# Optimization experiments

Measured on AMD Instinct MI355X. Metric: run time of the kernel, lower is better.

Reference implementation:

```python
import jax, jax.numpy as jnp
import numpy as np

VNUM = 50000
OUT = 128
E = 1600000
EPS = 1e-7


def setup_inputs() -> dict:
    key = jax.random.key(0)
    k = jax.random.split(key, 8)
    sidx = jax.random.randint(k[0], (E,), 0, VNUM, dtype=jnp.int64 if jax.config.jax_enable_x64 else jnp.int32)
    tidx = jax.random.randint(k[1], (E,), 0, VNUM, dtype=sidx.dtype)
    enorm = jax.random.uniform(k[2], (E,), dtype=jnp.float32)
    # edge signs +-1 as in signed graph conv
    esgn = jnp.where(jax.random.uniform(k[3], (E,)) < 0.5, -1.0, 1.0).astype(jnp.float32)
    # vrepr initialized trunc_normal(std=0.1) (zero_init=False)
    vrepr = 0.1 * jax.random.truncated_normal(k[4], -2.0, 2.0, (VNUM, OUT), dtype=jnp.float32)
    lim = 1.0 / np.sqrt(OUT)
    loc_w = jax.random.uniform(k[5], (OUT, OUT), jnp.float32, -lim, lim)
    loc_b = jnp.zeros((OUT,), jnp.float32)
    std_w = jax.random.uniform(k[6], (OUT, OUT), jnp.float32, -lim, lim)
    std_b = jnp.zeros((OUT,), jnp.float32)
    return {"sidx": sidx, "tidx": tidx, "enorm": enorm, "esgn": esgn,
            "vrepr": vrepr, "loc_w": loc_w, "loc_b": loc_b,
            "std_w": std_w, "std_b": std_b}


def reference(sidx, tidx, enorm, esgn, vrepr, loc_w, loc_b, std_w, std_b):
    # GraphConv: edge-weighted gather + scatter-add aggregation
    msg = vrepr[sidx] * (esgn * enorm)[:, None]          # [E, OUT]
    ptr = jax.ops.segment_sum(msg, tidx, num_segments=VNUM)  # [VNUM, OUT]
    loc = ptr @ loc_w.T + loc_b                          # Normal loc
    std = jax.nn.softplus(ptr @ std_w.T + std_b) + EPS   # Normal scale
    return loc, std
```

## Files before the change

kernel.cpp:

```cpp
#include <hip/hip_runtime.h>
#include <math.h>

#define VNUM 50000
#define OUTF 128
#define NEDGE 1600000
#define EPSF 1e-7f

#define CONV_BLOCKS 6250
#define BFRAG_BLOCKS 64

#define CHUNK 2048
#define NCB 49
#define COARSE_BLOCKS 782
#define BSTRIDE 36864
#define NSUB 4
#define FINE_BLOCKS (NCB * NSUB)

typedef __attribute__((ext_vector_type(8))) short short8;
typedef __attribute__((ext_vector_type(4))) float v4f;

__device__ __forceinline__ unsigned short f2bf(float f) {
    union { float f; unsigned int u; } c; c.f = f;
    unsigned int u = c.u;
    return (unsigned short)((u + 0x7FFFu + ((u >> 16) & 1u)) >> 16);
}
__device__ __forceinline__ float bf16_lo(unsigned int p) {
    union { unsigned int u; float f; } c; c.u = p << 16; return c.f;
}
__device__ __forceinline__ float bf16_hi(unsigned int p) {
    union { unsigned int u; float f; } c; c.u = p & 0xFFFF0000u; return c.f;
}

__device__ __forceinline__ int wave_incl_scan(int v, int lane) {
#pragma unroll
    for (int off = 1; off < 64; off <<= 1) {
        const int o = __shfl_up(v, off, 64);
        if (lane >= off) v += o;
    }
    return v;
}

__global__ __launch_bounds__(256) void prep_kernel(
    const float* __restrict__ vrepr, unsigned int* __restrict__ vrepr16,
    int* __restrict__ ccursor,
    const float* __restrict__ loc_w, const float* __restrict__ std_w,
    unsigned int* bfrag)
{
    const int b = blockIdx.x, tid = threadIdx.x;
    if (b < CONV_BLOCKS) {
        const size_t base = (size_t)b * 1024 + tid * 4;
        const float4 v = *reinterpret_cast<const float4*>(vrepr + base);
        uint2 o;
        o.x = (unsigned)f2bf(v.x) | ((unsigned)f2bf(v.y) << 16);
        o.y = (unsigned)f2bf(v.z) | ((unsigned)f2bf(v.w) << 16);
        *reinterpret_cast<uint2*>(vrepr16 + base / 2) = o;
    } else if (b == CONV_BLOCKS) {
        if (tid < NCB) ccursor[tid] = tid * BSTRIDE;
    } else {
        const int p = (b - (CONV_BLOCKS + 1)) * 256 + tid;
        const int j2 = p & 3, lq = (p >> 2) & 63, ks = (p >> 8) & 3, ct = p >> 10;
        const int k = ks * 32 + (lq >> 4) * 8 + j2 * 2;
        const int n = ct * 16 + (lq & 15);
        const float* wsrc = (n >> 7) ? std_w : loc_w;
        const int c = n & 127;
        bfrag[p] = (unsigned)f2bf(wsrc[c * 128 + k]) |
                   ((unsigned)f2bf(wsrc[c * 128 + k + 1]) << 16);
    }
}

__global__ __launch_bounds__(256) void coarse_kernel(
    const int* __restrict__ sidx, const int* __restrict__ tidx,
    const float* __restrict__ enorm, const float* __restrict__ esgn,
    int* __restrict__ ccursor, uint2* __restrict__ coarse8)
{
    __shared__ uint2 lrec[CHUNK];
    __shared__ int lcnt[4][NCB];
    __shared__ int lbase[4][NCB];
    __shared__ int loffs[NCB];
    __shared__ int grun[NCB];

    const int tid = threadIdx.x, lane = tid & 63, wv = tid >> 6;
    const int base = blockIdx.x * CHUNK;
    const int n = min(CHUNK, NEDGE - base);

    for (int i = tid; i < 4 * NCB; i += 256) (&lcnt[0][0])[i] = 0;
    __syncthreads();

    uint2 rec[8];
#pragma unroll
    for (int j = 0; j < 8; ++j) {
        const int e = base + j * 256 + tid;
        if (e < NEDGE) {
            const int t = tidx[e];
            const float w = esgn[e] * enorm[e];
            rec[j].x = ((unsigned)sidx[e] << 16) | (unsigned)f2bf(w);
            rec[j].y = (unsigned)t;
            atomicAdd(&lcnt[wv][t >> 10], 1);
        }
    }
    __syncthreads();

    if (tid < 64) {
        int c0 = 0, c1 = 0, c2 = 0, c3 = 0, tot = 0;
        if (lane < NCB) {
            c0 = lcnt[0][lane]; c1 = lcnt[1][lane];
            c2 = lcnt[2][lane]; c3 = lcnt[3][lane];
            tot = c0 + c1 + c2 + c3;
        }
        const int inc = wave_incl_scan(tot, lane);
        const int ex = inc - tot;
        if (lane < NCB) {
            loffs[lane]    = ex;
            lbase[0][lane] = ex;
            lbase[1][lane] = ex + c0;
            lbase[2][lane] = ex + c0 + c1;
            lbase[3][lane] = ex + c0 + c1 + c2;
            grun[lane] = atomicAdd(&ccursor[lane], tot);
        }
    }
    __syncthreads();

#pragma unroll
    for (int j = 0; j < 8; ++j) {
        const int e = base + j * 256 + tid;
        if (e < NEDGE) {
            const int cb = (int)(rec[j].y >> 10);
            const int pos = atomicAdd(&lbase[wv][cb], 1);
            lrec[pos] = rec[j];
        }
    }
    __syncthreads();

    for (int i = tid; i < n; i += 256) {
        const uint2 r = lrec[i];
        const int cb = (int)(r.y >> 10);
        coarse8[grun[cb] + (i - loffs[cb])] = r;
    }
}

__global__ __launch_bounds__(64) void scan_mid_kernel(
    const int* __restrict__ ccursor, int* __restrict__ cbase,
    int* __restrict__ offs)
{
    const int tid = threadIdx.x;
    const int len = (tid < NCB) ? (ccursor[tid] - tid * BSTRIDE) : 0;
    const int inc = wave_incl_scan(len, tid);
    const int ex = inc - len;
    if (tid < NCB) cbase[tid] = ex;
    if (tid == NCB - 1) { cbase[NCB] = inc; offs[VNUM] = inc; }
}

__global__ __launch_bounds__(1024) void hist_kernel(
    const uint2* __restrict__ coarse8, const int* __restrict__ cbase,
    int* __restrict__ hcnt)
{
    __shared__ int cnt[1024];
    const int tid = threadIdx.x;
    const int bin = blockIdx.x >> 2, s = blockIdx.x & 3;
    const int bs = bin * BSTRIDE;
    const int len = cbase[bin + 1] - cbase[bin];
    const int qs = bs + ((len * s) >> 2);
    const int qe = bs + ((len * (s + 1)) >> 2);
    cnt[tid] = 0;
    __syncthreads();
    for (int i = qs + tid; i < qe; i += 1024)
        atomicAdd(&cnt[coarse8[i].y & 1023], 1);
    __syncthreads();
    hcnt[blockIdx.x * 1024 + tid] = cnt[tid];
}

__global__ __launch_bounds__(1024) void scatter_fine_kernel(
    const uint2* __restrict__ coarse8, const int* __restrict__ cbase,
    const int* __restrict__ hcnt, int* __restrict__ offs,
    unsigned int* __restrict__ pairs)
{
    __shared__ int cur[1024];
    __shared__ int wsum[16];
    const int tid = threadIdx.x, lane = tid & 63, wv = tid >> 6;
    const int bin = blockIdx.x >> 2, s = blockIdx.x & 3;
    const int bs = bin * BSTRIDE;
    const int s0 = cbase[bin];
    const int len = cbase[bin + 1] - s0;
    const int qs = bs + ((len * s) >> 2);
    const int qe = bs + ((len * (s + 1)) >> 2);

    const int c0 = hcnt[(bin * 4 + 0) * 1024 + tid];
    const int c1 = hcnt[(bin * 4 + 1) * 1024 + tid];
    const int c2 = hcnt[(bin * 4 + 2) * 1024 + tid];
    const int c3 = hcnt[(bin * 4 + 3) * 1024 + tid];
    const int tot = c0 + c1 + c2 + c3;
    const int pre = (s > 0 ? c0 : 0) + (s > 1 ? c1 : 0) + (s > 2 ? c2 : 0);

    const int inc = wave_incl_scan(tot, lane);
    if (lane == 63) wsum[wv] = inc;
    __syncthreads();
    if (tid == 0) {
        int run = 0;
        for (int i = 0; i < 16; ++i) { const int t = wsum[i]; wsum[i] = run; run += t; }
    }
    __syncthreads();
    const int ex = s0 + wsum[wv] + inc - tot;
    const int gv = (bin << 10) + tid;
    if (s == 0 && gv < VNUM) offs[gv] = ex;
    cur[tid] = ex + pre;
    __syncthreads();

    for (int i = qs + tid; i < qe; i += 1024) {
        const uint2 r = coarse8[i];
        const int pos = atomicAdd(&cur[r.y & 1023], 1);
        pairs[pos] = r.x;
    }
}

__global__ __launch_bounds__(256) void aggregate_kernel(
    const int* __restrict__ offs, const unsigned int* __restrict__ pairs,
    const unsigned int* __restrict__ vrepr16, float* __restrict__ acc)
{
    const int v = blockIdx.x * 4 + (threadIdx.x >> 6);
    const int l = threadIdx.x & 63;
    int i = offs[v];
    const int end = offs[v + 1];

    float a0 = 0.0f, a1 = 0.0f;
    for (; i + 12 <= end; i += 12) {
        unsigned p[12], r[12];
#pragma unroll
        for (int j = 0; j < 12; ++j) p[j] = pairs[i + j];
#pragma unroll
        for (int j = 0; j < 12; ++j) r[j] = vrepr16[(size_t)(p[j] >> 16) * 64 + l];
#pragma unroll
        for (int j = 0; j < 12; ++j) {
            const float w = bf16_lo(p[j]);
            a0 = fmaf(bf16_lo(r[j]), w, a0);
            a1 = fmaf(bf16_hi(r[j]), w, a1);
        }
    }
    for (; i + 8 <= end; i += 8) {
        unsigned p[8], r[8];
#pragma unroll
        for (int j = 0; j < 8; ++j) p[j] = pairs[i + j];
#pragma unroll
        for (int j = 0; j < 8; ++j) r[j] = vrepr16[(size_t)(p[j] >> 16) * 64 + l];
#pragma unroll
        for (int j = 0; j < 8; ++j) {
            const float w = bf16_lo(p[j]);
            a0 = fmaf(bf16_lo(r[j]), w, a0);
            a1 = fmaf(bf16_hi(r[j]), w, a1);
        }
    }
    for (; i + 4 <= end; i += 4) {
        const unsigned p0 = pairs[i], p1 = pairs[i + 1];
        const unsigned p2 = pairs[i + 2], p3 = pairs[i + 3];
        const unsigned r0 = vrepr16[(size_t)(p0 >> 16) * 64 + l];
        const unsigned r1 = vrepr16[(size_t)(p1 >> 16) * 64 + l];
        const unsigned r2 = vrepr16[(size_t)(p2 >> 16) * 64 + l];
        const unsigned r3 = vrepr16[(size_t)(p3 >> 16) * 64 + l];
        const float w0 = bf16_lo(p0), w1 = bf16_lo(p1);
        const float w2 = bf16_lo(p2), w3 = bf16_lo(p3);
        a0 = fmaf(bf16_lo(r0), w0, a0); a1 = fmaf(bf16_hi(r0), w0, a1);
        a0 = fmaf(bf16_lo(r1), w1, a0); a1 = fmaf(bf16_hi(r1), w1, a1);
        a0 = fmaf(bf16_lo(r2), w2, a0); a1 = fmaf(bf16_hi(r2), w2, a1);
        a0 = fmaf(bf16_lo(r3), w3, a0); a1 = fmaf(bf16_hi(r3), w3, a1);
    }
    for (; i < end; ++i) {
        const unsigned p = pairs[i];
        const unsigned r = vrepr16[(size_t)(p >> 16) * 64 + l];
        const float w = bf16_lo(p);
        a0 = fmaf(bf16_lo(r), w, a0); a1 = fmaf(bf16_hi(r), w, a1);
    }
    *reinterpret_cast<float2*>(acc + (size_t)v * OUTF + 2 * l) = make_float2(a0, a1);
}

__global__ __launch_bounds__(256) void gemm_mfma_kernel(
    const float* acc, const unsigned int* __restrict__ bfrag,
    const float* __restrict__ loc_b, const float* __restrict__ std_b,
    float* out)
{
    __shared__ unsigned short tile[16][136];
    const int t = threadIdx.x;
    const int row0 = blockIdx.x * 16;
    const int l = t & 63, w = t >> 6;

    short8 bfr[4][4];
#pragma unroll
    for (int ct = 0; ct < 4; ++ct)
#pragma unroll
        for (int ks = 0; ks < 4; ++ks)
            bfr[ct][ks] = *reinterpret_cast<const short8*>(
                bfrag + ((((w * 4 + ct) * 4 + ks) * 64 + l) << 2));

    {
        const float* src = acc + (size_t)row0 * OUTF + t * 8;
        const float4 v0 = *reinterpret_cast<const float4*>(src);
        const float4 v1 = *reinterpret_cast<const float4*>(src + 4);
        uint4 pk;
        pk.x = (unsigned)f2bf(v0.x) | ((unsigned)f2bf(v0.y) << 16);
        pk.y = (unsigned)f2bf(v0.z) | ((unsigned)f2bf(v0.w) << 16);
        pk.z = (unsigned)f2bf(v1.x) | ((unsigned)f2bf(v1.y) << 16);
        pk.w = (unsigned)f2bf(v1.z) | ((unsigned)f2bf(v1.w) << 16);
        *reinterpret_cast<uint4*>(&tile[t >> 4][(t & 15) * 8]) = pk;
    }
    __syncthreads();

    const int m = l & 15, q = l >> 4;
    v4f accv[4];
#pragma unroll
    for (int ct = 0; ct < 4; ++ct) accv[ct] = (v4f){0.0f, 0.0f, 0.0f, 0.0f};

#pragma unroll
    for (int ks = 0; ks < 4; ++ks) {
        const short8 a = *reinterpret_cast<const short8*>(&tile[m][ks * 32 + q * 8]);
#pragma unroll
        for (int ct = 0; ct < 4; ++ct)
            accv[ct] = __builtin_amdgcn_mfma_f32_16x16x32_bf16(
                a, bfr[ct][ks], accv[ct], 0, 0, 0);
    }

#pragma unroll
    for (int ct = 0; ct < 4; ++ct) {
        const int colg = (w * 4 + ct) * 16 + m;
        const int h = colg >> 7, c = colg & 127;
        const float bias = (h ? std_b : loc_b)[c];
        float* dst = out + (h ? (size_t)VNUM * OUTF : (size_t)0);
#pragma unroll
        for (int reg = 0; reg < 4; ++reg) {
            const int row = row0 + q * 4 + reg;
            float x = accv[ct][reg] + bias;
            if (h) x = fmaxf(x, 0.0f) + log1pf(expf(-fabsf(x))) + EPSF;
            dst[(size_t)row * OUTF + c] = x;
        }
    }
}

__global__ __launch_bounds__(256) void gemm_fallback_kernel(
    const float* acc,
    const float* __restrict__ loc_w, const float* __restrict__ loc_b,
    const float* __restrict__ std_w, const float* __restrict__ std_b,
    float* out)
{
    __shared__ float tile[16][OUTF];
    const int t = threadIdx.x;
    const int row0 = blockIdx.x * 16;
    {
        const float4* src = reinterpret_cast<const float4*>(acc + (size_t)row0 * OUTF);
        float4* dst = reinterpret_cast<float4*>(&tile[0][0]);
        dst[t] = src[t]; dst[t + 256] = src[t + 256];
    }
    __syncthreads();
    const int is_std = t >> 7;
    const int c = t & 127;
    const float* w = (is_std ? std_w : loc_w) + (size_t)c * OUTF;
    const float bias = is_std ? std_b[c] : loc_b[c];
    float accv[16];
#pragma unroll
    for (int r = 0; r < 16; ++r) accv[r] = 0.0f;
    for (int k = 0; k < OUTF; k += 4) {
        const float4 wv = *reinterpret_cast<const float4*>(w + k);
#pragma unroll
        for (int r = 0; r < 16; ++r) {
            const float4 pv = *reinterpret_cast<const float4*>(&tile[r][k]);
            float a = accv[r];
            a = fmaf(pv.x, wv.x, a); a = fmaf(pv.y, wv.y, a);
            a = fmaf(pv.z, wv.z, a); a = fmaf(pv.w, wv.w, a);
            accv[r] = a;
        }
    }
    float* dst_base = out + (is_std ? (size_t)VNUM * OUTF : (size_t)0);
#pragma unroll
    for (int r = 0; r < 16; ++r) {
        const float x = accv[r] + bias;
        dst_base[(size_t)(row0 + r) * OUTF + c] =
            is_std ? (fmaxf(x, 0.0f) + log1pf(expf(-fabsf(x))) + EPSF) : x;
    }
}

extern "C" void kernel_launch(void* const* d_in, const int* in_sizes, int n_in,
                              void* d_out, int out_size, void* d_ws, size_t ws_size,
                              hipStream_t stream) {
    const int*   sidx  = (const int*)  d_in[0];
    const int*   tidx  = (const int*)  d_in[1];
    const float* enorm = (const float*)d_in[2];
    const float* esgn  = (const float*)d_in[3];
    const float* vrepr = (const float*)d_in[4];
    const float* loc_w = (const float*)d_in[5];
    const float* loc_b = (const float*)d_in[6];
    const float* std_w = (const float*)d_in[7];
    const float* std_b = (const float*)d_in[8];

    float* out = (float*)d_out;

    uint2* coarse8 = (uint2*)out;

    unsigned int* sbase   = (unsigned int*)(out + (size_t)VNUM * OUTF);
    unsigned int* pairs   = sbase;
    unsigned int* vrepr16 = sbase + NEDGE;
    int* offs    = (int*)(sbase + NEDGE + (size_t)VNUM * 64);
    int* cbase   = offs + VNUM + 1;
    int* ccursor = cbase + NCB + 1;
    int* hcnt    = ccursor + NCB;

    const bool use_ws = ws_size >= 16384 * sizeof(unsigned int);
    unsigned int* bfrag = use_ws ? (unsigned int*)d_ws : nullptr;

    const int prep_blocks = CONV_BLOCKS + 1 + (use_ws ? BFRAG_BLOCKS : 0);
    prep_kernel       <<<prep_blocks, 256, 0, stream>>>(vrepr, vrepr16, ccursor,
                                                        loc_w, std_w, bfrag);
    coarse_kernel     <<<COARSE_BLOCKS, 256, 0, stream>>>(sidx, tidx, enorm, esgn,
                                                          ccursor, coarse8);
    scan_mid_kernel   <<<1, 64, 0, stream>>>(ccursor, cbase, offs);
    hist_kernel       <<<FINE_BLOCKS, 1024, 0, stream>>>(coarse8, cbase, hcnt);
    scatter_fine_kernel<<<FINE_BLOCKS, 1024, 0, stream>>>(coarse8, cbase, hcnt,
                                                          offs, pairs);

    float* acc = out;
    aggregate_kernel<<<VNUM / 4, 256, 0, stream>>>(offs, pairs, vrepr16, acc);

    if (use_ws) {
        gemm_mfma_kernel<<<VNUM / 16, 256, 0, stream>>>(acc, bfrag, loc_b, std_b, out);
    } else {
        gemm_fallback_kernel<<<VNUM / 16, 256, 0, stream>>>(acc, loc_w, loc_b,
                                                            std_w, std_b, out);
    }
}
```

Before: 231.7 us.

## Drop scan kernel, write aggregate as packed bf16, use nontemporal loads

Removes the single-block scan_mid kernel: each scatter_fine block recomputes the bucket prefix from ccursor with a wave scan, and prep writes offs[VNUM]=NEDGE directly. The aggregate kernel now converts its accumulators to packed bf16 and stores them with nontemporal stores, so the GEMM reads half as many bytes and skips its own conversion. Pair loads use nontemporal loads, and the 8-wide unrolled loop is dropped. This saves one launch and some memory traffic. In exchange, every scatter block repeats the small scan, and the rounding to bf16 moves to the aggregate kernel's store.

```diff
diff --git a/kernel.cpp b/kernel.cpp
--- a/kernel.cpp
+++ b/kernel.cpp
@@ -42,7 +42,7 @@
 
 __global__ __launch_bounds__(256) void prep_kernel(
     const float* __restrict__ vrepr, unsigned int* __restrict__ vrepr16,
-    int* __restrict__ ccursor,
+    int* __restrict__ ccursor, int* __restrict__ offs,
     const float* __restrict__ loc_w, const float* __restrict__ std_w,
     unsigned int* bfrag)
 {
@@ -56,6 +56,7 @@
         *reinterpret_cast<uint2*>(vrepr16 + base / 2) = o;
     } else if (b == CONV_BLOCKS) {
         if (tid < NCB) ccursor[tid] = tid * BSTRIDE;
+        if (tid == 63) offs[VNUM] = NEDGE;
     } else {
         const int p = (b - (CONV_BLOCKS + 1)) * 256 + tid;
         const int j2 = p & 3, lq = (p >> 2) & 63, ks = (p >> 8) & 3, ct = p >> 10;
@@ -138,27 +139,15 @@
     }
 }
 
-__global__ __launch_bounds__(64) void scan_mid_kernel(
-    const int* __restrict__ ccursor, int* __restrict__ cbase,
-    int* __restrict__ offs)
-{
-    const int tid = threadIdx.x;
-    const int len = (tid < NCB) ? (ccursor[tid] - tid * BSTRIDE) : 0;
-    const int inc = wave_incl_scan(len, tid);
-    const int ex = inc - len;
-    if (tid < NCB) cbase[tid] = ex;
-    if (tid == NCB - 1) { cbase[NCB] = inc; offs[VNUM] = inc; }
-}
-
 __global__ __launch_bounds__(1024) void hist_kernel(
-    const uint2* __restrict__ coarse8, const int* __restrict__ cbase,
+    const uint2* __restrict__ coarse8, const int* __restrict__ ccursor,
     int* __restrict__ hcnt)
 {
     __shared__ int cnt[1024];
     const int tid = threadIdx.x;
     const int bin = blockIdx.x >> 2, s = blockIdx.x & 3;
     const int bs = bin * BSTRIDE;
-    const int len = cbase[bin + 1] - cbase[bin];
+    const int len = ccursor[bin] - bs;
     const int qs = bs + ((len * s) >> 2);
     const int qe = bs + ((len * (s + 1)) >> 2);
     cnt[tid] = 0;
@@ -170,17 +159,24 @@
 }
 
 __global__ __launch_bounds__(1024) void scatter_fine_kernel(
-    const uint2* __restrict__ coarse8, const int* __restrict__ cbase,
+    const uint2* __restrict__ coarse8, const int* __restrict__ ccursor,
     const int* __restrict__ hcnt, int* __restrict__ offs,
     unsigned int* __restrict__ pairs)
 {
     __shared__ int cur[1024];
     __shared__ int wsum[16];
+    __shared__ int sh_s0;
     const int tid = threadIdx.x, lane = tid & 63, wv = tid >> 6;
     const int bin = blockIdx.x >> 2, s = blockIdx.x & 3;
     const int bs = bin * BSTRIDE;
-    const int s0 = cbase[bin];
-    const int len = cbase[bin + 1] - s0;
+
+    if (tid < 64) {
+        const int lenl = (tid < NCB) ? (ccursor[tid] - tid * BSTRIDE) : 0;
+        const int incc = wave_incl_scan(lenl, tid);
+        if (tid == bin) sh_s0 = incc - lenl;
+    }
+
+    const int len = ccursor[bin] - bs;
     const int qs = bs + ((len * s) >> 2);
     const int qe = bs + ((len * (s + 1)) >> 2);
 
@@ -199,6 +195,7 @@
         for (int i = 0; i < 16; ++i) { const int t = wsum[i]; wsum[i] = run; run += t; }
     }
     __syncthreads();
+    const int s0 = sh_s0;
     const int ex = s0 + wsum[wv] + inc - tot;
     const int gv = (bin << 10) + tid;
     if (s == 0 && gv < VNUM) offs[gv] = ex;
@@ -214,7 +211,7 @@
 
 __global__ __launch_bounds__(256) void aggregate_kernel(
     const int* __restrict__ offs, const unsigned int* __restrict__ pairs,
-    const unsigned int* __restrict__ vrepr16, float* __restrict__ acc)
+    const unsigned int* __restrict__ vrepr16, unsigned int* __restrict__ accu)
 {
     const int v = blockIdx.x * 4 + (threadIdx.x >> 6);
     const int l = threadIdx.x & 63;
@@ -225,7 +222,7 @@
     for (; i + 12 <= end; i += 12) {
         unsigned p[12], r[12];
 #pragma unroll
-        for (int j = 0; j < 12; ++j) p[j] = pairs[i + j];
+        for (int j = 0; j < 12; ++j) p[j] = __builtin_nontemporal_load(pairs + i + j);
 #pragma unroll
         for (int j = 0; j < 12; ++j) r[j] = vrepr16[(size_t)(p[j] >> 16) * 64 + l];
 #pragma unroll
@@ -235,44 +232,31 @@
             a1 = fmaf(bf16_hi(r[j]), w, a1);
         }
     }
-    for (; i + 8 <= end; i += 8) {
-        unsigned p[8], r[8];
-#pragma unroll
-        for (int j = 0; j < 8; ++j) p[j] = pairs[i + j];
-#pragma unroll
-        for (int j = 0; j < 8; ++j) r[j] = vrepr16[(size_t)(p[j] >> 16) * 64 + l];
-#pragma unroll
-        for (int j = 0; j < 8; ++j) {
+    for (; i + 4 <= end; i += 4) {
+        unsigned p[4], r[4];
+#pragma unroll
+        for (int j = 0; j < 4; ++j) p[j] = __builtin_nontemporal_load(pairs + i + j);
+#pragma unroll
+        for (int j = 0; j < 4; ++j) r[j] = vrepr16[(size_t)(p[j] >> 16) * 64 + l];
+#pragma unroll
+        for (int j = 0; j < 4; ++j) {
             const float w = bf16_lo(p[j]);
             a0 = fmaf(bf16_lo(r[j]), w, a0);
             a1 = fmaf(bf16_hi(r[j]), w, a1);
         }
     }
-    for (; i + 4 <= end; i += 4) {
-        const unsigned p0 = pairs[i], p1 = pairs[i + 1];
-        const unsigned p2 = pairs[i + 2], p3 = pairs[i + 3];
-        const unsigned r0 = vrepr16[(size_t)(p0 >> 16) * 64 + l];
-        const unsigned r1 = vrepr16[(size_t)(p1 >> 16) * 64 + l];
-        const unsigned r2 = vrepr16[(size_t)(p2 >> 16) * 64 + l];
-        const unsigned r3 = vrepr16[(size_t)(p3 >> 16) * 64 + l];
-        const float w0 = bf16_lo(p0), w1 = bf16_lo(p1);
-        const float w2 = bf16_lo(p2), w3 = bf16_lo(p3);
-        a0 = fmaf(bf16_lo(r0), w0, a0); a1 = fmaf(bf16_hi(r0), w0, a1);
-        a0 = fmaf(bf16_lo(r1), w1, a0); a1 = fmaf(bf16_hi(r1), w1, a1);
-        a0 = fmaf(bf16_lo(r2), w2, a0); a1 = fmaf(bf16_hi(r2), w2, a1);
-        a0 = fmaf(bf16_lo(r3), w3, a0); a1 = fmaf(bf16_hi(r3), w3, a1);
-    }
     for (; i < end; ++i) {
-        const unsigned p = pairs[i];
+        const unsigned p = __builtin_nontemporal_load(pairs + i);
         const unsigned r = vrepr16[(size_t)(p >> 16) * 64 + l];
         const float w = bf16_lo(p);
         a0 = fmaf(bf16_lo(r), w, a0); a1 = fmaf(bf16_hi(r), w, a1);
     }
-    *reinterpret_cast<float2*>(acc + (size_t)v * OUTF + 2 * l) = make_float2(a0, a1);
+    const unsigned pk = (unsigned)f2bf(a0) | ((unsigned)f2bf(a1) << 16);
+    __builtin_nontemporal_store(pk, accu + (size_t)v * 128 + l);
 }
 
 __global__ __launch_bounds__(256) void gemm_mfma_kernel(
-    const float* acc, const unsigned int* __restrict__ bfrag,
+    const unsigned int* accu, const unsigned int* __restrict__ bfrag,
     const float* __restrict__ loc_b, const float* __restrict__ std_b,
     float* out)
 {
@@ -290,15 +274,9 @@
                 bfrag + ((((w * 4 + ct) * 4 + ks) * 64 + l) << 2));
 
     {
-        const float* src = acc + (size_t)row0 * OUTF + t * 8;
-        const float4 v0 = *reinterpret_cast<const float4*>(src);
-        const float4 v1 = *reinterpret_cast<const float4*>(src + 4);
-        uint4 pk;
-        pk.x = (unsigned)f2bf(v0.x) | ((unsigned)f2bf(v0.y) << 16);
-        pk.y = (unsigned)f2bf(v0.z) | ((unsigned)f2bf(v0.w) << 16);
-        pk.z = (unsigned)f2bf(v1.x) | ((unsigned)f2bf(v1.y) << 16);
-        pk.w = (unsigned)f2bf(v1.z) | ((unsigned)f2bf(v1.w) << 16);
-        *reinterpret_cast<uint4*>(&tile[t >> 4][(t & 15) * 8]) = pk;
+        const uint4 av = *reinterpret_cast<const uint4*>(
+            accu + (size_t)(row0 + (t >> 4)) * 128 + (t & 15) * 4);
+        *reinterpret_cast<uint4*>(&tile[t >> 4][(t & 15) * 8]) = av;
     }
     __syncthreads();
 
@@ -333,7 +311,7 @@
 }
 
 __global__ __launch_bounds__(256) void gemm_fallback_kernel(
-    const float* acc,
+    const unsigned int* accu,
     const float* __restrict__ loc_w, const float* __restrict__ loc_b,
     const float* __restrict__ std_w, const float* __restrict__ std_b,
     float* out)
@@ -342,9 +320,13 @@
     const int t = threadIdx.x;
     const int row0 = blockIdx.x * 16;
     {
-        const float4* src = reinterpret_cast<const float4*>(acc + (size_t)row0 * OUTF);
-        float4* dst = reinterpret_cast<float4*>(&tile[0][0]);
-        dst[t] = src[t]; dst[t + 256] = src[t + 256];
+        const uint4 av = *reinterpret_cast<const uint4*>(
+            accu + (size_t)(row0 + (t >> 4)) * 128 + (t & 15) * 4);
+        float* dst = &tile[t >> 4][(t & 15) * 8];
+        dst[0] = bf16_lo(av.x); dst[1] = bf16_hi(av.x);
+        dst[2] = bf16_lo(av.y); dst[3] = bf16_hi(av.y);
+        dst[4] = bf16_lo(av.z); dst[5] = bf16_hi(av.z);
+        dst[6] = bf16_lo(av.w); dst[7] = bf16_hi(av.w);
     }
     __syncthreads();
     const int is_std = t >> 7;
@@ -390,35 +372,32 @@
     float* out = (float*)d_out;
 
     uint2* coarse8 = (uint2*)out;
+    unsigned int* accu = (unsigned int*)out;
 
     unsigned int* sbase   = (unsigned int*)(out + (size_t)VNUM * OUTF);
     unsigned int* pairs   = sbase;
     unsigned int* vrepr16 = sbase + NEDGE;
     int* offs    = (int*)(sbase + NEDGE + (size_t)VNUM * 64);
-    int* cbase   = offs + VNUM + 1;
-    int* ccursor = cbase + NCB + 1;
+    int* ccursor = offs + VNUM + 1;
     int* hcnt    = ccursor + NCB;
 
     const bool use_ws = ws_size >= 16384 * sizeof(unsigned int);
     unsigned int* bfrag = use_ws ? (unsigned int*)d_ws : nullptr;
 
     const int prep_blocks = CONV_BLOCKS + 1 + (use_ws ? BFRAG_BLOCKS : 0);
-    prep_kernel       <<<prep_blocks, 256, 0, stream>>>(vrepr, vrepr16, ccursor,
-                                                        loc_w, std_w, bfrag);
-    coarse_kernel     <<<COARSE_BLOCKS, 256, 0, stream>>>(sidx, tidx, enorm, esgn,
-                                                          ccursor, coarse8);
-    scan_mid_kernel   <<<1, 64, 0, stream>>>(ccursor, cbase, offs);
-    hist_kernel       <<<FINE_BLOCKS, 1024, 0, stream>>>(coarse8, cbase, hcnt);
-    scatter_fine_kernel<<<FINE_BLOCKS, 1024, 0, stream>>>(coarse8, cbase, hcnt,
+    prep_kernel        <<<prep_blocks, 256, 0, stream>>>(vrepr, vrepr16, ccursor,
+                                                         offs, loc_w, std_w, bfrag);
+    coarse_kernel      <<<COARSE_BLOCKS, 256, 0, stream>>>(sidx, tidx, enorm, esgn,
+                                                           ccursor, coarse8);
+    hist_kernel        <<<FINE_BLOCKS, 1024, 0, stream>>>(coarse8, ccursor, hcnt);
+    scatter_fine_kernel<<<FINE_BLOCKS, 1024, 0, stream>>>(coarse8, ccursor, hcnt,
                                                           offs, pairs);
-
-    float* acc = out;
-    aggregate_kernel<<<VNUM / 4, 256, 0, stream>>>(offs, pairs, vrepr16, acc);
+    aggregate_kernel   <<<VNUM / 4, 256, 0, stream>>>(offs, pairs, vrepr16, accu);
 
     if (use_ws) {
-        gemm_mfma_kernel<<<VNUM / 16, 256, 0, stream>>>(acc, bfrag, loc_b, std_b, out);
+        gemm_mfma_kernel<<<VNUM / 16, 256, 0, stream>>>(accu, bfrag, loc_b, std_b, out);
     } else {
-        gemm_fallback_kernel<<<VNUM / 16, 256, 0, stream>>>(acc, loc_w, loc_b,
+        gemm_fallback_kernel<<<VNUM / 16, 256, 0, stream>>>(accu, loc_w, loc_b,
                                                             std_w, std_b, out);
     }
 }
```

Result: no change. 230.6 us (-0.5%).
